# Optimization experiments

Measured on AMD Instinct MI355X. Metric: run time of the kernel, lower is better.

## Reference

```python
import jax, jax.numpy as jnp
import numpy as np

B, S, W = 32, 128, 16
E, CD, H, P = 256, 64, 512, 256
V, CV, NC = 50000, 256, 6
CK, WK = 8, 64  # merged char/word conv kernel sizes


def conv1d(x, w, b):
    # x: [N, Cin, L], w: [Cout, Cin, K] -> [N, Cout, L-K+1] (VALID)
    y = jax.lax.conv_general_dilated(x, w, (1,), 'VALID',
                                     dimension_numbers=('NCH', 'OIH', 'NCH'))
    return y + b[None, :, None]


def setup_inputs() -> dict:
    key = jax.random.key(0)
    ks = iter(jax.random.split(key, 40))
    nrm = lambda shape: jax.random.normal(next(ks), shape, dtype=jnp.float32) * 0.05
    return {
        'seq': jax.random.randint(next(ks), (B, S), 0, V),
        'seq_char': jax.random.randint(next(ks), (B, S, W), 0, CV),
        'classes': jnp.arange(NC, dtype=jnp.int32).reshape(NC, 1),
        'embed_w': nrm((V, E)),
        'char_embed_w': nrm((CV, CD)),
        'class_embed_w': nrm((NC, E)),
        'char_conv_w': nrm((CD, CD, CK)), 'char_conv_b': nrm((CD,)),
        'word_conv_w': nrm((E, E + CD, WK)), 'word_conv_b': nrm((E,)),
        'f_Wih': nrm((4 * H, E + CD)), 'f_Whh': nrm((4 * H, H)), 'f_b': nrm((4 * H,)),
        'b_Wih': nrm((4 * H, E + CD)), 'b_Whh': nrm((4 * H, H)), 'b_b': nrm((4 * H,)),
        'attend': nrm((E, 2 * H)),
        'd_Wih': nrm((6 * H, E + 2 * H)), 'd_Whh': nrm((6 * H, 2 * H)),
        'd_bih': nrm((6 * H,)), 'd_bhh': nrm((6 * H,)),
        'proj_w': nrm((P, 2 * H)), 'proj_b': nrm((P,)),
        'cls_w': nrm((2, P)), 'cls_b': nrm((2,)),
    }


def reference(seq, seq_char, classes, embed_w, char_embed_w, class_embed_w,
              char_conv_w, char_conv_b, word_conv_w, word_conv_b,
              f_Wih, f_Whh, f_b, b_Wih, b_Whh, b_b, attend,
              d_Wih, d_Whh, d_bih, d_bhh, proj_w, proj_b, cls_w, cls_b):
    # eval-mode forward (dropout p=0.01 is identity at eval time)
    Bq, Sq = seq.shape
    pad_mask = (seq > 0).astype(jnp.float32)            # [B,S]
    word_e = jnp.tanh(embed_w[seq])                     # [B,S,E]
    # char CNN: all char convs share kernel size -> merged into one conv
    ce = char_embed_w[seq_char]                         # [B,S,W,CD]
    ce = ce.reshape(Bq * Sq, W, CD).transpose(0, 2, 1)  # [B*S, CD, W]
    char_feat = jnp.tanh(conv1d(ce, char_conv_w, char_conv_b).mean(-1).reshape(Bq, Sq, CD))
    x = jnp.concatenate([word_e, char_feat], -1)        # [B,S,E+CD]
    # word CNN over full sequence -> [B,E]
    conv_seq = jnp.tanh(conv1d(x.transpose(0, 2, 1), word_conv_w, word_conv_b).mean(-1))
    # BiLSTM; backward direction uses seq_emb[-i], i.e. order [0, S-1, ..., 1] (as in original)
    xs = x.transpose(1, 0, 2)                           # [S,B,E+CD]
    xs_b = xs[(-jnp.arange(Sq)) % Sq]

    def lstm_scan(Wih, Whh, b, inputs):
        def step(carry, xt):
            h, c = carry
            g = xt @ Wih.T + h @ Whh.T + b
            i, f, gg, o = jnp.split(g, 4, axis=-1)
            c = jax.nn.sigmoid(f) * c + jax.nn.sigmoid(i) * jnp.tanh(gg)
            h = jax.nn.sigmoid(o) * jnp.tanh(c)
            return (h, c), h
        h0 = jnp.zeros((Bq, H), x.dtype)
        _, hs = jax.lax.scan(step, (h0, h0), inputs)
        return hs

    fouts = lstm_scan(f_Wih, f_Whh, f_b, xs)            # [S,B,H]
    bouts = lstm_scan(b_Wih, b_Whh, b_b, xs_b)[::-1]    # reversed, as in original
    seq_repr = jnp.concatenate([fouts, bouts], -1)      # [S,B,2H]
    h0 = seq_repr[-1]                                   # decoder init state [B,2H]
    seq_repr = seq_repr.transpose(1, 0, 2)              # [B,S,2H]
    # class attention: the expanded attn rows are identical across positions,
    # so sum over dim 1 of the [B,S,S] bmm equals S * tanh(a_c) . seq_repr[b,t]
    a = jnp.tanh(jnp.tanh(class_embed_w[classes[:, 0]])) @ attend   # [C,2H]
    scores = Sq * jnp.einsum('ch,bth->cbt', jnp.tanh(a), seq_repr)  # [C,B,S]
    scores = scores * pad_mask[None]
    att_ctx = jnp.einsum('cbt,bth->cbh', jnp.tanh(scores), seq_repr)  # [C,B,2H]

    def gru_step(h, ctx):
        inp = jnp.concatenate([conv_seq, ctx], -1)      # [B, E+2H]
        gi = inp @ d_Wih.T + d_bih
        gh = h @ d_Whh.T + d_bhh
        ir, iz, inn = jnp.split(gi, 3, -1)
        hr, hz, hn = jnp.split(gh, 3, -1)
        r = jax.nn.sigmoid(ir + hr)
        z = jax.nn.sigmoid(iz + hz)
        n = jnp.tanh(inn + r * hn)
        h_new = jnp.tanh((1 - z) * n + z * h)           # post-tanh state fed back (as in original)
        logits = (h_new @ proj_w.T + proj_b) @ cls_w.T + cls_b
        return h_new, jax.nn.log_softmax(logits, -1)

    _, outs = jax.lax.scan(gru_step, h0, att_ctx)       # [C,B,2]
    return outs
```

## Files before the change

### kernel.cpp

```cpp
#include <hip/hip_runtime.h>

typedef __bf16 bf16_t;
typedef __bf16 bf16x8 __attribute__((ext_vector_type(8)));
typedef float f32x4 __attribute__((ext_vector_type(4)));
typedef unsigned u32x4 __attribute__((ext_vector_type(4)));
typedef unsigned long long u64;

static constexpr int BB = 32, SS = 128, WW = 16, EE = 256, CDm = 64, HH = 512, PP = 256;
static constexpr int EC = 320;
static constexpr int H2 = 1024;
static constexpr int G6 = 3072;
static constexpr int NKT = 28;
static constexpr int NKTX = 12;

__device__ __forceinline__ float sigm(float x){ return 1.f/(1.f + expf(-x)); }

#define ALOAD(p)    __hip_atomic_load((p),  __ATOMIC_RELAXED, __HIP_MEMORY_SCOPE_AGENT)
#define ASTORE(p,v) __hip_atomic_store((p),(v),__ATOMIC_RELAXED, __HIP_MEMORY_SCOPE_AGENT)

template<bool LLC>
__device__ __forceinline__ unsigned ld_flag(const unsigned* p){
  unsigned r;
  if constexpr (LLC)
    asm volatile("global_load_dword %0, %1, off sc0 sc1\n\ts_waitcnt vmcnt(0)"
                 : "=&v"(r) : "v"(p) : "memory");
  else
    asm volatile("global_load_dword %0, %1, off sc0\n\ts_waitcnt vmcnt(0)"
                 : "=&v"(r) : "v"(p) : "memory");
  return r;
}
template<bool LLC>
__device__ __forceinline__ void ld16(u32x4& d, const void* p){
  if constexpr (LLC)
    asm volatile("global_load_dwordx4 %0, %1, off sc0 sc1" : "=&v"(d) : "v"(p) : "memory");
  else
    asm volatile("global_load_dwordx4 %0, %1, off sc0"     : "=&v"(d) : "v"(p) : "memory");
}
template<bool LLC>
__device__ __forceinline__ void st32(unsigned* p, unsigned v){
  if constexpr (LLC)
    asm volatile("global_store_dword %0, %1, off sc0 sc1" :: "v"(p), "v"(v) : "memory");
  else
    asm volatile("global_store_dword %0, %1, off sc0"     :: "v"(p), "v"(v) : "memory");
}
__device__ __forceinline__ void vm_drain(){
  asm volatile("s_waitcnt vmcnt(0)" ::: "memory");
  __builtin_amdgcn_sched_barrier(0);
}

__global__ void k_embed(const int* __restrict__ seq, const float* __restrict__ embed_w,
                        float* __restrict__ x, float* __restrict__ mask){
  int bs = blockIdx.x; int c = threadIdx.x;
  int wid = seq[bs];
  x[(size_t)bs*EC + c] = tanhf(embed_w[(size_t)wid*EE + c]);
  if (c == 0) mask[bs] = (wid > 0) ? 1.f : 0.f;
}

__global__ void k_cbar(const int* __restrict__ seq_char, const float* __restrict__ cemb,
                       float* __restrict__ cbar){
  int bs = blockIdx.x; int c = threadIdx.x;
  float ce[WW];
  #pragma unroll
  for (int p = 0; p < WW; ++p){
    int id = seq_char[bs*WW + p];
    ce[p] = cemb[(size_t)id*CDm + c];
  }
  #pragma unroll
  for (int k = 0; k < 8; ++k){
    float s = 0.f;
    #pragma unroll
    for (int p = 0; p < 9; ++p) s += ce[k+p];
    cbar[(size_t)bs*512 + c*8 + k] = s * (1.f/9.f);
  }
}

__global__ __launch_bounds__(64) void k_xbar(const float* __restrict__ x, float* __restrict__ xbar){
  __shared__ float xl[64][129];
  int gid = blockIdx.x*64 + threadIdx.x;
  int b = gid / EC, c = gid % EC;
  int tl = threadIdx.x;
  for (int t = 0; t < SS; ++t) xl[tl][t] = x[((size_t)b*SS + t)*EC + c];
  float s = 0.f;
  for (int t = 0; t < 65; ++t) s += xl[tl][t];
  const float inv = 1.f/65.f;
  float* o = &xbar[(size_t)(b*EC + c)*64];
  o[0] = s*inv;
  for (int k = 1; k < 64; ++k){ s += xl[tl][k+64] - xl[tl][k-1]; o[k] = s*inv; }
}

template<int BM,int BN,int TM,int TN>
__global__ __launch_bounds__(256) void k_gemm(const float* __restrict__ A,
    const float* __restrict__ Wm, float* __restrict__ part,
    int M, int N, int K, int kslice){
  __shared__ float As[32][BM+4];
  __shared__ float Ws[32][BN+4];
  const int tid = threadIdx.x;
  const int tx = tid & 15, ty = tid >> 4;
  const int m0 = blockIdx.x*BM, n0 = blockIdx.y*BN, ks = blockIdx.z;
  const int kb = ks*kslice;
  float acc[TM][TN];
  #pragma unroll
  for (int i = 0; i < TM; ++i)
    #pragma unroll
    for (int j = 0; j < TN; ++j) acc[i][j] = 0.f;
  for (int kt = 0; kt < kslice; kt += 32){
    constexpr int AIT = (BM*8)/256;
    #pragma unroll
    for (int it = 0; it < AIT; ++it){
      int ch = tid + it*256;
      int r = ch >> 3, kc = (ch & 7)*4;
      float4 v = *(const float4*)(A + (size_t)(m0+r)*K + kb + kt + kc);
      As[kc+0][r]=v.x; As[kc+1][r]=v.y; As[kc+2][r]=v.z; As[kc+3][r]=v.w;
    }
    constexpr int WIT = (BN*8)/256;
    #pragma unroll
    for (int it = 0; it < WIT; ++it){
      int ch = tid + it*256;
      int r = ch >> 3, kc = (ch & 7)*4;
      float4 v = *(const float4*)(Wm + (size_t)(n0+r)*K + kb + kt + kc);
      Ws[kc+0][r]=v.x; Ws[kc+1][r]=v.y; Ws[kc+2][r]=v.z; Ws[kc+3][r]=v.w;
    }
    __syncthreads();
    #pragma unroll
    for (int kk = 0; kk < 32; ++kk){
      float a[TM], wv[TN];
      #pragma unroll
      for (int i = 0; i < TM; ++i) a[i] = As[kk][ty*TM+i];
      #pragma unroll
      for (int j = 0; j < TN; ++j) wv[j] = Ws[kk][tx*TN+j];
      #pragma unroll
      for (int i = 0; i < TM; ++i)
        #pragma unroll
        for (int j = 0; j < TN; ++j) acc[i][j] = fmaf(a[i], wv[j], acc[i][j]);
    }
    __syncthreads();
  }
  #pragma unroll
  for (int i = 0; i < TM; ++i){
    int row = m0 + ty*TM + i;
    #pragma unroll
    for (int j = 0; j < TN; ++j){
      int col = n0 + tx*TN + j;
      part[((size_t)ks*M + row)*N + col] = acc[i][j];
    }
  }
}

__global__ __launch_bounds__(64) void k_fin(const float* __restrict__ part,
    const float* __restrict__ bias, float* __restrict__ out,
    int M, int N, int KS, int ldc, int act){
  int col = blockIdx.x*64 + threadIdx.x;
  int row = blockIdx.y;
  float v = bias ? bias[col] : 0.f;
  for (int ks = 0; ks < KS; ++ks) v += part[((size_t)ks*M + row)*N + col];
  if (act) v = tanhf(v);
  out[(size_t)row*ldc + col] = v;
}

__global__ __launch_bounds__(64) void k_packw(const float* __restrict__ fWih, const float* __restrict__ fWhh,
    const float* __restrict__ bWih, const float* __restrict__ bWhh, bf16_t* __restrict__ Wp){
  int id = blockIdx.x;
  int kt = id % NKT; id /= NKT;
  int slice = id % 32; int dir = id / 32;
  int l = threadIdx.x;
  const float* Whh = dir ? bWhh : fWhh;
  const float* Wih = dir ? bWih : fWih;
  int krow = (l >> 4)*8;
  for (int nt = 0; nt < 4; ++nt){
    int row = nt*512 + slice*16 + (l & 15);
    bf16_t* dst = &Wp[((((size_t)(dir*32+slice)*NKT + kt)*4 + nt)*64 + l)*8];
    if (kt < 16){
      const float* src = &Whh[(size_t)row*512 + kt*32 + krow];
      #pragma unroll
      for (int r = 0; r < 8; ++r) dst[r] = (bf16_t)src[r];
    } else {
      int kx = (kt-16)*32 + krow;
      if (kx + 8 <= 320){
        const float* src = &Wih[(size_t)row*320 + kx];
        #pragma unroll
        for (int r = 0; r < 8; ++r) dst[r] = (bf16_t)src[r];
      } else {
        #pragma unroll
        for (int r = 0; r < 8; ++r) dst[r] = (bf16_t)0.f;
      }
    }
  }
}

__global__ __launch_bounds__(64) void k_packdw(const float* __restrict__ W, bf16_t* __restrict__ Wo){
  int id = blockIdx.x;
  int kt = id % 32; id /= 32;
  int nt = id % 3;  int wg = id / 3;
  int l = threadIdx.x;
  int col = nt*1024 + wg*16 + (l & 15);
  int k0 = kt*32 + (l >> 4)*8;
  bf16_t* dst = Wo + (((size_t)(wg*3 + nt)*32 + kt)*64 + l)*8;
  const float* src = W + (size_t)col*1024 + k0;
  #pragma unroll
  for (int r = 0; r < 8; ++r) dst[r] = (bf16_t)src[r];
}

__global__ __launch_bounds__(64) void k_packpw(const float* __restrict__ W, bf16_t* __restrict__ Wo){
  int id = blockIdx.x;
  int kt = id & 31, wg = id >> 5;
  int l = threadIdx.x;
  int col = wg*16 + (l & 15);
  int k0 = kt*32 + (l >> 4)*8;
  bf16_t* dst = Wo + (((size_t)wg*32 + kt)*64 + l)*8;
  const float* src = W + (size_t)col*1024 + k0;
  #pragma unroll
  for (int r = 0; r < 8; ++r) dst[r] = (bf16_t)src[r];
}

__global__ __launch_bounds__(64) void k_packx(const float* __restrict__ x, bf16_t* __restrict__ xp){
  int id = blockIdx.x;
  int ktx = id % NKTX; id /= NKTX;
  int mt = id & 1; int t = id >> 1;
  int l = threadIdx.x;
  int b = (l & 15) + 16*mt;
  int c = ktx*32 + (l >> 4)*8;
  bf16_t* dst = &xp[(((size_t)t*2 + mt)*NKTX + ktx)*64*8 + (size_t)l*8];
  if (c + 8 <= EC){
    const float* src = &x[((size_t)b*SS + t)*EC + c];
    #pragma unroll
    for (int r = 0; r < 8; ++r) dst[r] = (bf16_t)src[r];
  } else {
    #pragma unroll
    for (int r = 0; r < 8; ++r) dst[r] = (bf16_t)0.f;
  }
}

__global__ __launch_bounds__(256) void k_zero(unsigned int* __restrict__ base, int n){
  int i = blockIdx.x*256 + threadIdx.x;
  if (i < n) ASTORE(base + i, 0u);
}

__global__ __launch_bounds__(64) void k_hprep(const float* __restrict__ seq_repr,
                                              bf16_t* __restrict__ hdp){
  int mt = blockIdx.x >> 5, kt = blockIdx.x & 31, l = threadIdx.x;
  int b = mt*16 + (l & 15);
  int jb = kt*32 + (l >> 4)*8;
  const float* src = &seq_repr[((size_t)b*SS + 127)*H2 + jb];
  unsigned* dst = (unsigned*)(hdp + (((size_t)mt*32 + kt)*64 + l)*8);
  #pragma unroll
  for (int p = 0; p < 4; ++p){
    unsigned pk = (unsigned)__builtin_bit_cast(unsigned short, (bf16_t)src[2*p])
                | ((unsigned)__builtin_bit_cast(unsigned short, (bf16_t)src[2*p+1]) << 16);
    ASTORE(dst + p, pk);
  }
}

template<bool LLC>
__device__ void lstm_body(const bf16_t* __restrict__ Wp, const bf16_t* __restrict__ xp,
    bf16_t* __restrict__ hp, const float* __restrict__ fb, const float* __restrict__ bb,
    float* __restrict__ seq_repr, unsigned* __restrict__ lf,
    int dir, int slice, int tid, bf16_t* Wl, float (*red)[32][65],
    float* bias_l, float (*c_l)[32]){
  const int wv = tid >> 6, lane = tid & 63;
  {
    const uint4* src = (const uint4*)(Wp + ((size_t)(dir*32 + slice))*NKT*4*64*8);
    uint4* dst = (uint4*)Wl;
    for (int i = tid; i < NKT*4*64*8/8; i += 256) dst[i] = src[i];
  }
  if (tid < 64){
    const float* bv = dir ? bb : fb;
    bias_l[tid] = bv[(tid >> 4)*512 + slice*16 + (tid & 15)];
  }
  ((float*)c_l)[tid]       = 0.f;
  ((float*)c_l)[tid + 256] = 0.f;
  __syncthreads();

  for (int t = 0; t < SS; ++t){
    const int ph = t & 1;
    const int s = dir ? ((SS - t) & 127) : t;
    f32x4 acc[2][4];
    f32x4 zero = {0.f,0.f,0.f,0.f};
    #pragma unroll
    for (int m = 0; m < 2; ++m)
      #pragma unroll
      for (int n = 0; n < 4; ++n) acc[m][n] = zero;

    const bf16_t* xb = xp + (size_t)s*2*NKTX*64*8;
    bf16x8 ax[3][2];
    #pragma unroll
    for (int i = 0; i < 3; ++i){
      int ktx = wv*3 + i;
      #pragma unroll
      for (int m = 0; m < 2; ++m)
        ax[i][m] = *reinterpret_cast<const bf16x8*>(xb + (((size_t)m*NKTX + ktx)*64 + lane)*8);
    }
    #pragma unroll
    for (int i = 0; i < 3; ++i){
      int kt = 16 + wv*3 + i;
      #pragma unroll
      for (int nt = 0; nt < 4; ++nt){
        bf16x8 Bf = *reinterpret_cast<const bf16x8*>(&Wl[(((size_t)kt*4 + nt)*64 + lane)*8]);
        acc[0][nt] = __builtin_amdgcn_mfma_f32_16x16x32_bf16(ax[i][0], Bf, acc[0][nt], 0, 0, 0);
        acc[1][nt] = __builtin_amdgcn_mfma_f32_16x16x32_bf16(ax[i][1], Bf, acc[1][nt], 0, 0, 0);
      }
    }
    if (t > 0 && lane < 8){
      int prod = dir*32 + (wv + 4*(lane >> 1))*2 + (lane & 1);
      const unsigned* fp = lf + prod*16;
      unsigned tgt = (unsigned)t;
      for(;;){
        unsigned v = ld_flag<LLC>(fp);
        if (__ballot(v < tgt) == 0ull) break;
      }
    }
    const bf16_t* hb_ = hp + ((size_t)(ph*2 + dir))*2*16*64*8;
    u32x4 hr[4][2];
    #pragma unroll
    for (int i = 0; i < 4; ++i){
      int kt = wv + 4*i;
      #pragma unroll
      for (int m = 0; m < 2; ++m)
        ld16<LLC>(hr[i][m], hb_ + (((size_t)m*16 + kt)*64 + lane)*8);
    }
    vm_drain();
    #pragma unroll
    for (int i = 0; i < 4; ++i){
      int kt = wv + 4*i;
      bf16x8 a0 = __builtin_bit_cast(bf16x8, hr[i][0]);
      bf16x8 a1 = __builtin_bit_cast(bf16x8, hr[i][1]);
      #pragma unroll
      for (int nt = 0; nt < 4; ++nt){
        bf16x8 Bf = *reinterpret_cast<const bf16x8*>(&Wl[(((size_t)kt*4 + nt)*64 + lane)*8]);
        acc[0][nt] = __builtin_amdgcn_mfma_f32_16x16x32_bf16(a0, Bf, acc[0][nt], 0, 0, 0);
        acc[1][nt] = __builtin_amdgcn_mfma_f32_16x16x32_bf16(a1, Bf, acc[1][nt], 0, 0, 0);
      }
    }
    {
      int r0 = (lane >> 4)*4, cc = lane & 15;
      #pragma unroll
      for (int m = 0; m < 2; ++m)
        #pragma unroll
        for (int n = 0; n < 4; ++n)
          #pragma unroll
          for (int e = 0; e < 4; ++e)
            red[wv][m*16 + r0 + e][n*16 + cc] = acc[m][n][e];
    }
    __syncthreads();
    {
      int b = tid & 31, jjp = tid >> 5;
      float hv[2];
      #pragma unroll
      for (int u2 = 0; u2 < 2; ++u2){
        int jj = jjp*2 + u2;
        float gi_ = bias_l[jj],     gf_ = bias_l[16+jj];
        float gg_ = bias_l[32+jj],  go_ = bias_l[48+jj];
        #pragma unroll
        for (int w2 = 0; w2 < 4; ++w2){
          gi_ += red[w2][b][jj];      gf_ += red[w2][b][16+jj];
          gg_ += red[w2][b][32+jj];   go_ += red[w2][b][48+jj];
        }
        float ii = sigm(gi_), ff = sigm(gf_), g2 = tanhf(gg_), oo = sigm(go_);
        float c = ff*c_l[jj][b] + ii*g2;
        c_l[jj][b] = c;
        hv[u2] = oo*tanhf(c);
      }
      int j0 = slice*16 + jjp*2;
      int s_out = dir ? (127 - t) : t;
      float2 st; st.x = hv[0]; st.y = hv[1];
      *(float2*)&seq_repr[((size_t)b*SS + s_out)*H2 + dir*HH + j0] = st;
      int mt = b >> 4, kth = j0 >> 5, ln = (b & 15) + 16*((j0 >> 3) & 3), rg = j0 & 7;
      unsigned pk = (unsigned)__builtin_bit_cast(unsigned short, (bf16_t)hv[0])
                  | ((unsigned)__builtin_bit_cast(unsigned short, (bf16_t)hv[1]) << 16);
      unsigned* dst = (unsigned*)(hp +
          ((((size_t)((ph^1)*2 + dir)*2 + mt)*16 + kth)*64 + ln)*8 + rg);
      st32<LLC>(dst, pk);
    }
    asm volatile("s_waitcnt vmcnt(0)" ::: "memory");
    __syncthreads();
    if (tid == 0)
      st32<LLC>(lf + (dir*32 + slice)*16, (unsigned)(t+1));
  }
}

__global__ __launch_bounds__(256, 1) void k_lstm(const bf16_t* __restrict__ Wp,
    const bf16_t* __restrict__ xp, bf16_t* __restrict__ hp,
    const float* __restrict__ fb, const float* __restrict__ bb,
    float* __restrict__ seq_repr, unsigned* __restrict__ lf,
    unsigned* __restrict__ xcc_tab, unsigned* __restrict__ modep){
  const int blk = blockIdx.x;
  const int tid = threadIdx.x;
  __shared__ __align__(16) bf16_t Wl[NKT*4*64*8];
  __shared__ float red[4][32][65];
  __shared__ float bias_l[64];
  __shared__ float c_l[16][32];
  __shared__ unsigned mode_s;

  unsigned xcc;
  asm volatile("s_getreg_b32 %0, hwreg(HW_REG_XCC_ID)" : "=s"(xcc));
  if (tid == 0) ASTORE(xcc_tab + blk, xcc + 1u);
  if (blk == 0){
    unsigned* tabl = (unsigned*)red;
    unsigned v = 0; int spins = 0;
    for (;;){
      v = ALOAD(xcc_tab + tid);
      if (v != 0u || spins >= 200000) break;
      ++spins; __builtin_amdgcn_s_sleep(2);
    }
    tabl[tid] = v;
    __syncthreads();
    if (tid == 0){
      unsigned mode = 1;
      unsigned c0 = tabl[0], c1 = tabl[1];
      if (c0 == 0u || c1 == 0u) mode = 2;
      for (int k = 0; k < 32; ++k)
        if (tabl[8*k] != c0 || tabl[8*k + 1] != c1) mode = 2;
      ASTORE(modep, mode);
      mode_s = mode;
    }
    __syncthreads();
  } else {
    if (tid == 0){
      unsigned m;
      while ((m = ALOAD(modep)) == 0u) __builtin_amdgcn_s_sleep(2);
      mode_s = m;
    }
    __syncthreads();
  }
  const unsigned mode = mode_s;
  int dir, slice; bool worker;
  if (mode == 1){ worker = (blk & 7) < 2; dir = blk & 7; slice = blk >> 3; }
  else          { worker = blk < 64;      dir = blk >> 5; slice = blk & 31; }
  if (!worker) return;
  if (mode == 1)
    lstm_body<false>(Wp, xp, hp, fb, bb, seq_repr, lf, dir, slice, tid, Wl, red, bias_l, c_l);
  else
    lstm_body<true >(Wp, xp, hp, fb, bb, seq_repr, lf, dir, slice, tid, Wl, red, bias_l, c_l);
}

__global__ __launch_bounds__(256) void k_ta(const int* __restrict__ classes,
    const float* __restrict__ cls_emb, const float* __restrict__ attend, float* __restrict__ ta){
  int c = blockIdx.x;
  __shared__ float t2[EE];
  int tid = threadIdx.x;
  int ci = classes[c];
  t2[tid] = tanhf(tanhf(cls_emb[(size_t)ci*EE + tid]));
  __syncthreads();
  for (int r = 0; r < 4; ++r){
    int h = r*256 + tid;
    float acc = 0.f;
    for (int e = 0; e < EE; ++e) acc = fmaf(t2[e], attend[(size_t)e*H2 + h], acc);
    ta[c*H2 + h] = tanhf(acc);
  }
}

__global__ __launch_bounds__(256) void k_ctx(const float* __restrict__ ta,
    const float* __restrict__ seq_repr, const float* __restrict__ mask, float* __restrict__ ctx){
  int c = blockIdx.x, b = blockIdx.y;
  __shared__ float ta_l[H2];
  __shared__ float ps[128][2];
  __shared__ float sc[128];
  int tid = threadIdx.x;
  for (int i = tid; i < H2; i += 256) ta_l[i] = ta[c*H2 + i];
  __syncthreads();
  {
    int tt = tid >> 1, half = tid & 1;
    const float* row = &seq_repr[((size_t)b*SS + tt)*H2 + half*512];
    const float* tl = &ta_l[half*512];
    float p = 0.f;
    for (int i = 0; i < 512; i += 4){
      float4 v = *(const float4*)&row[i];
      p = fmaf(tl[i], v.x, p);   p = fmaf(tl[i+1], v.y, p);
      p = fmaf(tl[i+2], v.z, p); p = fmaf(tl[i+3], v.w, p);
    }
    ps[tt][half] = p;
  }
  __syncthreads();
  if (tid < 128){
    float s = (ps[tid][0] + ps[tid][1]) * 128.f * mask[b*SS + tid];
    sc[tid] = tanhf(s);
  }
  __syncthreads();
  {
    int h = tid*4;
    float4 a = {0.f,0.f,0.f,0.f};
    for (int t = 0; t < SS; ++t){
      float s = sc[t];
      float4 v = *(const float4*)&seq_repr[((size_t)b*SS + t)*H2 + h];
      a.x = fmaf(s, v.x, a.x); a.y = fmaf(s, v.y, a.y);
      a.z = fmaf(s, v.z, a.z); a.w = fmaf(s, v.w, a.w);
    }
    *(float4*)&ctx[((size_t)c*BB + b)*H2 + h] = a;
  }
}

__global__ void k_inp(const float* __restrict__ conv_seq, const float* __restrict__ ctx,
                      float* __restrict__ inp){
  int cb = blockIdx.x;
  int b = cb & 31;
  for (int k = threadIdx.x; k < 1280; k += 256){
    float v = (k < 256) ? conv_seq[b*256 + k] : ctx[(size_t)cb*H2 + (k - 256)];
    inp[(size_t)cb*1280 + k] = v;
  }
}

__global__ __launch_bounds__(256, 1) void k_dec(
    const bf16_t* __restrict__ Whp, const bf16_t* __restrict__ Ppw,
    const float* __restrict__ gi, const float* __restrict__ d_bhh,
    const float* __restrict__ seq_repr,
    const float* __restrict__ proj_b, const float* __restrict__ cls_w,
    const float* __restrict__ cls_b, bf16_t* __restrict__ hdp,
    float* __restrict__ pl, unsigned int* __restrict__ dfh,
    unsigned int* __restrict__ dfpl, float* __restrict__ out){
  const int wg = blockIdx.x;
  const int tid = threadIdx.x;
  const int wv = tid >> 6, lane = tid & 63;
  __shared__ __align__(16) bf16_t Wl[3*32*64*8];
  __shared__ float red[4][32][49];
  __shared__ float plred[8][32][2];
  __shared__ float cv[2];
  {
    const uint4* src = (const uint4*)(Whp + (size_t)wg*3*32*64*8);
    uint4* dst = (uint4*)Wl;
    for (int i = tid; i < 3*32*64*8/8; i += 256) dst[i] = src[i];
  }
  const int b = tid & 31, jp = tid >> 5;
  const int j0 = wg*16 + jp*2;
  float hold[2];
  hold[0] = seq_repr[((size_t)b*SS + 127)*H2 + j0];
  hold[1] = seq_repr[((size_t)b*SS + 127)*H2 + j0 + 1];
  float bhh[3][2];
  #pragma unroll
  for (int g = 0; g < 3; ++g){
    bhh[g][0] = d_bhh[g*1024 + j0];
    bhh[g][1] = d_bhh[g*1024 + j0 + 1];
  }
  __syncthreads();
  union HU { unsigned long long u[2]; bf16x8 v; };
  const int r0 = (lane >> 4)*4, cc = lane & 15;

  for (int c = 0; c < 6; ++c){
    if (c > 0){
      const unsigned int* fp = dfh + lane*16;
      unsigned tgt = (unsigned)c;
      for(;;){
        unsigned v = ALOAD(fp);
        if (__ballot(v < tgt) == 0ull) break;
      }
    }
    f32x4 acc[2][3];
    f32x4 zero = {0.f,0.f,0.f,0.f};
    #pragma unroll
    for (int m = 0; m < 2; ++m)
      #pragma unroll
      for (int n = 0; n < 3; ++n) acc[m][n] = zero;
    const bf16_t* hb = hdp + (size_t)(c & 1)*2*32*64*8;
    #pragma unroll
    for (int i = 0; i < 8; ++i){
      int kt = wv*8 + i;
      HU u0, u1;
      const unsigned long long* p0 = (const unsigned long long*)(hb + (((size_t)0*32 + kt)*64 + lane)*8);
      const unsigned long long* p1 = (const unsigned long long*)(hb + (((size_t)1*32 + kt)*64 + lane)*8);
      u0.u[0] = ALOAD(p0);     u0.u[1] = ALOAD(p0 + 1);
      u1.u[0] = ALOAD(p1);     u1.u[1] = ALOAD(p1 + 1);
      #pragma unroll
      for (int nt = 0; nt < 3; ++nt){
        bf16x8 Bf = *reinterpret_cast<const bf16x8*>(&Wl[(((size_t)nt*32 + kt)*64 + lane)*8]);
        acc[0][nt] = __builtin_amdgcn_mfma_f32_16x16x32_bf16(u0.v, Bf, acc[0][nt], 0, 0, 0);
        acc[1][nt] = __builtin_amdgcn_mfma_f32_16x16x32_bf16(u1.v, Bf, acc[1][nt], 0, 0, 0);
      }
    }
    #pragma unroll
    for (int m = 0; m < 2; ++m)
      #pragma unroll
      for (int n = 0; n < 3; ++n)
        #pragma unroll
        for (int e = 0; e < 4; ++e)
          red[wv][m*16 + r0 + e][n*16 + cc] = acc[m][n][e];
    __syncthreads();
    float hnew[2];
    #pragma unroll
    for (int u2 = 0; u2 < 2; ++u2){
      int jj = jp*2 + u2;
      float r_ = 0.f, z_ = 0.f, n_ = 0.f;
      #pragma unroll
      for (int w = 0; w < 4; ++w){
        r_ += red[w][b][jj]; z_ += red[w][b][16+jj]; n_ += red[w][b][32+jj];
      }
      const float* gr = gi + ((size_t)(c*BB) + b)*G6 + wg*16 + jj;
      float rr = sigm(gr[0]    + bhh[0][u2] + r_);
      float zz = sigm(gr[1024] + bhh[1][u2] + z_);
      float nn = tanhf(gr[2048] + rr*(bhh[2][u2] + n_));
      hnew[u2] = tanhf((1.f - zz)*nn + zz*hold[u2]);
      hold[u2] = hnew[u2];
    }
    {
      int kt = j0 >> 5, ln = (b & 15) + 16*((j0 >> 3) & 3), rg = j0 & 7, mt = b >> 4;
      unsigned pk = (unsigned)__builtin_bit_cast(unsigned short, (bf16_t)hnew[0])
                  | ((unsigned)__builtin_bit_cast(unsigned short, (bf16_t)hnew[1]) << 16);
      unsigned* dst = (unsigned*)(hdp + (size_t)((c+1)&1)*2*32*64*8 +
                                  (((size_t)(mt*32 + kt)*64 + ln)*8 + rg));
      ASTORE(dst, pk);
    }
    __syncthreads();
    if (tid == 0)
      ASTORE(dfh + wg*16, (unsigned)(c+1));
    if (wg < 16){
      {
        const unsigned int* fp = dfh + lane*16;
        unsigned tgt = (unsigned)(c+1);
        for(;;){
          unsigned v = ALOAD(fp);
          if (__ballot(v < tgt) == 0ull) break;
        }
      }
      f32x4 pacc[2] = {zero, zero};
      const bf16_t* hb2 = hdp + (size_t)((c+1)&1)*2*32*64*8;
      #pragma unroll
      for (int i = 0; i < 8; ++i){
        int kt = wv*8 + i;
        HU u0, u1;
        const unsigned long long* p0 = (const unsigned long long*)(hb2 + (((size_t)0*32 + kt)*64 + lane)*8);
        const unsigned long long* p1 = (const unsigned long long*)(hb2 + (((size_t)1*32 + kt)*64 + lane)*8);
        u0.u[0] = ALOAD(p0);     u0.u[1] = ALOAD(p0 + 1);
        u1.u[0] = ALOAD(p1);     u1.u[1] = ALOAD(p1 + 1);
        bf16x8 Bf = *reinterpret_cast<const bf16x8*>(Ppw + (((size_t)wg*32 + kt)*64 + lane)*8);
        pacc[0] = __builtin_amdgcn_mfma_f32_16x16x32_bf16(u0.v, Bf, pacc[0], 0, 0, 0);
        pacc[1] = __builtin_amdgcn_mfma_f32_16x16x32_bf16(u1.v, Bf, pacc[1], 0, 0, 0);
      }
      #pragma unroll
      for (int m = 0; m < 2; ++m)
        #pragma unroll
        for (int e = 0; e < 4; ++e)
          red[wv][m*16 + r0 + e][cc] = pacc[m][e];
      __syncthreads();
      {
        int colp = tid >> 5;
        float v0 = 0.f, v1 = 0.f;
        #pragma unroll
        for (int w = 0; w < 4; ++w){
          v0 += red[w][b][colp*2];
          v1 += red[w][b][colp*2+1];
        }
        int c0 = wg*16 + colp*2, c1 = c0 + 1;
        plred[colp][b][0] = v0*cls_w[c0]      + v1*cls_w[c1];
        plred[colp][b][1] = v0*cls_w[PP + c0] + v1*cls_w[PP + c1];
      }
      __syncthreads();
      if (tid < 32){
        float s0 = 0.f, s1 = 0.f;
        #pragma unroll
        for (int g = 0; g < 8; ++g){ s0 += plred[g][tid][0]; s1 += plred[g][tid][1]; }
        unsigned* dp = (unsigned*)(pl + (((size_t)c*16 + wg)*32 + tid)*2);
        ASTORE(dp,     __builtin_bit_cast(unsigned, s0));
        ASTORE(dp + 1, __builtin_bit_cast(unsigned, s1));
      }
      __syncthreads();
      if (tid == 0)
        ASTORE(dfpl + wg*16, (unsigned)(c+1));
    }
  }
  if (wg == 0){
    if (lane < 16){
      const unsigned int* fp = dfpl + lane*16;
      for(;;){
        unsigned v = ALOAD(fp);
        if (__ballot(v < 6u) == 0ull) break;
      }
    }
    __syncthreads();
    float* cr = (float*)red;
    cr[tid*2]   = proj_b[tid]*cls_w[tid];
    cr[tid*2+1] = proj_b[tid]*cls_w[PP + tid];
    __syncthreads();
    if (tid < 2){
      float s = 0.f;
      for (int i = 0; i < 256; ++i) s += cr[i*2 + tid];
      cv[tid] = s;
    }
    __syncthreads();
    if (tid < 32){
      for (int c = 0; c < 6; ++c){
        float a0 = cv[0] + cls_b[0], a1 = cv[1] + cls_b[1];
        for (int w = 0; w < 16; ++w){
          const unsigned* dp = (const unsigned*)(pl + (((size_t)c*16 + w)*32 + tid)*2);
          a0 += __builtin_bit_cast(float, ALOAD(dp));
          a1 += __builtin_bit_cast(float, ALOAD(dp + 1));
        }
        float mx = fmaxf(a0, a1);
        float ls = mx + logf(expf(a0 - mx) + expf(a1 - mx));
        out[((size_t)c*BB + tid)*2 + 0] = a0 - ls;
        out[((size_t)c*BB + tid)*2 + 1] = a1 - ls;
      }
    }
  }
}

extern "C" void kernel_launch(void* const* d_in, const int* in_sizes, int n_in,
                              void* d_out, int out_size, void* d_ws, size_t ws_size,
                              hipStream_t stream){
  const int*   seq          = (const int*)  d_in[0];
  const int*   seq_char     = (const int*)  d_in[1];
  const int*   classes      = (const int*)  d_in[2];
  const float* embed_w      = (const float*)d_in[3];
  const float* char_embed_w = (const float*)d_in[4];
  const float* class_embed_w= (const float*)d_in[5];
  const float* char_conv_w  = (const float*)d_in[6];
  const float* char_conv_b  = (const float*)d_in[7];
  const float* word_conv_w  = (const float*)d_in[8];
  const float* word_conv_b  = (const float*)d_in[9];
  const float* f_Wih = (const float*)d_in[10];
  const float* f_Whh = (const float*)d_in[11];
  const float* f_b   = (const float*)d_in[12];
  const float* b_Wih = (const float*)d_in[13];
  const float* b_Whh = (const float*)d_in[14];
  const float* b_b   = (const float*)d_in[15];
  const float* attend = (const float*)d_in[16];
  const float* d_Wih  = (const float*)d_in[17];
  const float* d_Whh  = (const float*)d_in[18];
  const float* d_bih  = (const float*)d_in[19];
  const float* d_bhh  = (const float*)d_in[20];
  const float* proj_w = (const float*)d_in[21];
  const float* proj_b = (const float*)d_in[22];
  const float* cls_w  = (const float*)d_in[23];
  const float* cls_b  = (const float*)d_in[24];
  float* out = (float*)d_out;

  char* wsb = (char*)d_ws;
  size_t off = 0;
  auto alloc = [&](size_t bytes) -> char* {
    char* p = wsb + off;
    off += (bytes + 255) & ~(size_t)255;
    return p;
  };
  unsigned int* flags = (unsigned int*)alloc(12288);
  unsigned int* lf   = flags;
  unsigned int* dfh  = flags + 1024;
  unsigned int* dfpl = flags + 2048;
  unsigned int* xcc_tab = (unsigned int*)alloc(1024);
  unsigned int* modep   = (unsigned int*)alloc(256);
  bf16_t* hp  = (bf16_t*)alloc((size_t)2*2*2*16*64*8 * 2);
  const int ZERO_DWORDS = 3072 + 256 + 64 + 32768;
  bf16_t* hdp = (bf16_t*)alloc((size_t)2*2*32*64*8 * 2);
  bf16_t* Wp  = (bf16_t*)alloc((size_t)2*32*NKT*4*64*8 * 2);
  bf16_t* Whp = (bf16_t*)alloc((size_t)64*3*32*64*8 * 2);
  bf16_t* Ppw = (bf16_t*)alloc((size_t)16*32*64*8 * 2);
  bf16_t* xp  = (bf16_t*)alloc((size_t)128*2*NKTX*64*8 * 2);
  float* pl       = (float*)alloc((size_t)6*16*32*2*4);
  float* x        = (float*)alloc((size_t)BB*SS*EC*4);
  float* mask     = (float*)alloc((size_t)BB*SS*4);
  float* cbar     = (float*)alloc((size_t)4096*512*4);
  float* xbar     = (float*)alloc((size_t)BB*EC*64*4);
  float* conv_seq = (float*)alloc((size_t)BB*256*4);
  float* seq_repr = (float*)alloc((size_t)BB*SS*H2*4);
  float* ta       = (float*)alloc((size_t)6*H2*4);
  float* ctx      = (float*)alloc((size_t)6*BB*H2*4);
  float* inp      = (float*)alloc((size_t)192*1280*4);
  float* gi       = (float*)alloc((size_t)192*G6*4);
  float* part_char= (float*)alloc((size_t)2*4096*64*4);
  float* part_word= (float*)alloc((size_t)32*BB*256*4);
  float* part_gi  = (float*)alloc((size_t)4*192*G6*4);
  (void)ws_size; (void)in_sizes; (void)n_in; (void)out_size;

  k_zero<<<(ZERO_DWORDS + 255)/256, 256, 0, stream>>>((unsigned int*)d_ws, ZERO_DWORDS);

  k_packw<<<2*32*NKT, 64, 0, stream>>>(f_Wih, f_Whh, b_Wih, b_Whh, Wp);
  k_packdw<<<64*3*32, 64, 0, stream>>>(d_Whh, Whp);
  k_packpw<<<16*32, 64, 0, stream>>>(proj_w, Ppw);
  k_embed<<<BB*SS, 256, 0, stream>>>(seq, embed_w, x, mask);
  k_cbar<<<BB*SS, 64, 0, stream>>>(seq_char, char_embed_w, cbar);
  k_gemm<32,64,2,4><<<dim3(128,1,2), 256, 0, stream>>>(cbar, char_conv_w, part_char, 4096, 64, 512, 256);
  k_fin<<<dim3(1,4096), 64, 0, stream>>>(part_char, char_conv_b, x + 256, 4096, 64, 2, EC, 1);
  k_xbar<<<160, 64, 0, stream>>>(x, xbar);
  k_gemm<32,64,2,4><<<dim3(1,4,32), 256, 0, stream>>>(xbar, word_conv_w, part_word, 32, 256, 20480, 640);
  k_fin<<<dim3(4,32), 64, 0, stream>>>(part_word, word_conv_b, conv_seq, 32, 256, 32, 256, 1);
  k_packx<<<128*2*NKTX, 64, 0, stream>>>(x, xp);
  k_lstm<<<256, 256, 0, stream>>>(Wp, xp, hp, f_b, b_b, seq_repr, lf, xcc_tab, modep);
  k_ta<<<6, 256, 0, stream>>>(classes, class_embed_w, attend, ta);
  k_ctx<<<dim3(6,32), 256, 0, stream>>>(ta, seq_repr, mask, ctx);
  k_inp<<<192, 256, 0, stream>>>(conv_seq, ctx, inp);
  k_gemm<64,64,4,4><<<dim3(3,48,4), 256, 0, stream>>>(inp, d_Wih, part_gi, 192, G6, 1280, 320);
  k_fin<<<dim3(48,192), 64, 0, stream>>>(part_gi, d_bih, gi, 192, G6, 4, G6, 0);
  k_hprep<<<64, 64, 0, stream>>>(seq_repr, hdp);
  k_dec<<<64, 256, 0, stream>>>(Whp, Ppw, gi, d_bhh, seq_repr, proj_b, cls_w, cls_b,
                                hdp, pl, dfh, dfpl, out);
}
```

Before: 645.1 us.

## Restructure LSTM recurrence into 128 single-wave workgroups with wave-local gating

The bidirectional LSTM kernel now runs as 128 one-wave workgroups, each owning 8 hidden units per direction, instead of 64 four-wave blocks with 16 units each. Each wave computes the full K reduction itself, so the cross-wave shared-memory reduction and __syncthreads per step go away, and the cell state stays in registers. The XCC-detection mode switch and its non-LLC path are removed: all flag and h loads/stores now use system-coherent sc0 sc1, and the spin-wait adds s_sleep. The trade-off is waiting on 64 producer flags per step instead of 16, and a serial 28-tile MFMA chain in a single wave.

Result: slower. 1.007 ms (+56.2%).

```diff
diff --git a/kernel.cpp b/kernel.cpp
--- a/kernel.cpp
+++ b/kernel.cpp
@@ -18,30 +18,20 @@
 #define ALOAD(p)    __hip_atomic_load((p),  __ATOMIC_RELAXED, __HIP_MEMORY_SCOPE_AGENT)
 #define ASTORE(p,v) __hip_atomic_store((p),(v),__ATOMIC_RELAXED, __HIP_MEMORY_SCOPE_AGENT)
 
-template<bool LLC>
 __device__ __forceinline__ unsigned ld_flag(const unsigned* p){
   unsigned r;
-  if constexpr (LLC)
-    asm volatile("global_load_dword %0, %1, off sc0 sc1\n\ts_waitcnt vmcnt(0)"
-                 : "=&v"(r) : "v"(p) : "memory");
-  else
-    asm volatile("global_load_dword %0, %1, off sc0\n\ts_waitcnt vmcnt(0)"
-                 : "=&v"(r) : "v"(p) : "memory");
+  asm volatile("global_load_dword %0, %1, off sc0 sc1\n\ts_waitcnt vmcnt(0)"
+               : "=&v"(r) : "v"(p) : "memory");
   return r;
 }
-template<bool LLC>
 __device__ __forceinline__ void ld16(u32x4& d, const void* p){
-  if constexpr (LLC)
-    asm volatile("global_load_dwordx4 %0, %1, off sc0 sc1" : "=&v"(d) : "v"(p) : "memory");
-  else
-    asm volatile("global_load_dwordx4 %0, %1, off sc0"     : "=&v"(d) : "v"(p) : "memory");
-}
-template<bool LLC>
-__device__ __forceinline__ void st32(unsigned* p, unsigned v){
-  if constexpr (LLC)
-    asm volatile("global_store_dword %0, %1, off sc0 sc1" :: "v"(p), "v"(v) : "memory");
-  else
-    asm volatile("global_store_dword %0, %1, off sc0"     :: "v"(p), "v"(v) : "memory");
+  asm volatile("global_load_dwordx4 %0, %1, off sc0 sc1" : "=&v"(d) : "v"(p) : "memory");
+}
+__device__ __forceinline__ void st16(void* p, u32x4 v){
+  asm volatile("global_store_dwordx4 %0, %1, off sc0 sc1" :: "v"(p), "v"(v) : "memory");
+}
+__device__ __forceinline__ void st32c(unsigned* p, unsigned v){
+  asm volatile("global_store_dword %0, %1, off sc0 sc1" :: "v"(p), "v"(v) : "memory");
 }
 __device__ __forceinline__ void vm_drain(){
   asm volatile("s_waitcnt vmcnt(0)" ::: "memory");
@@ -157,18 +147,19 @@
   out[(size_t)row*ldc + col] = v;
 }
 
-__global__ __launch_bounds__(64) void k_packw(const float* __restrict__ fWih, const float* __restrict__ fWhh,
-    const float* __restrict__ bWih, const float* __restrict__ bWhh, bf16_t* __restrict__ Wp){
+__global__ __launch_bounds__(64) void k_packw2(const float* __restrict__ fWih, const float* __restrict__ fWhh,
+    const float* __restrict__ bWih, const float* __restrict__ bWhh, bf16_t* __restrict__ Wp2){
   int id = blockIdx.x;
   int kt = id % NKT; id /= NKT;
-  int slice = id % 32; int dir = id / 32;
+  int ub = id % 64; int dir = id / 64;
   int l = threadIdx.x;
   const float* Whh = dir ? bWhh : fWhh;
   const float* Wih = dir ? bWih : fWih;
+  int cl = l & 15, ul = cl >> 2, g = cl & 3;
   int krow = (l >> 4)*8;
-  for (int nt = 0; nt < 4; ++nt){
-    int row = nt*512 + slice*16 + (l & 15);
-    bf16_t* dst = &Wp[((((size_t)(dir*32+slice)*NKT + kt)*4 + nt)*64 + l)*8];
+  for (int nt = 0; nt < 2; ++nt){
+    int row = g*512 + ub*8 + nt*4 + ul;
+    bf16_t* dst = &Wp2[((((size_t)(dir*64+ub)*NKT + kt)*2 + nt)*64 + l)*8];
     if (kt < 16){
       const float* src = &Whh[(size_t)row*512 + kt*32 + krow];
       #pragma unroll
@@ -250,186 +241,123 @@
   }
 }
 
-template<bool LLC>
-__device__ void lstm_body(const bf16_t* __restrict__ Wp, const bf16_t* __restrict__ xp,
-    bf16_t* __restrict__ hp, const float* __restrict__ fb, const float* __restrict__ bb,
-    float* __restrict__ seq_repr, unsigned* __restrict__ lf,
-    int dir, int slice, int tid, bf16_t* Wl, float (*red)[32][65],
-    float* bias_l, float (*c_l)[32]){
-  const int wv = tid >> 6, lane = tid & 63;
+__global__ __launch_bounds__(64, 1) void k_lstm(const bf16_t* __restrict__ Wp2,
+    const bf16_t* __restrict__ xp, bf16_t* __restrict__ hp,
+    const float* __restrict__ fb, const float* __restrict__ bb,
+    float* __restrict__ seq_repr, unsigned* __restrict__ lf){
+  const int wg = blockIdx.x;
+  const int dir = wg >> 6, ub = wg & 63;
+  const int lane = threadIdx.x;
+  __shared__ __align__(16) bf16_t Wl[NKT*2*64*8];
+  __shared__ float red[32*33 + 1];
+  __shared__ __align__(16) bf16_t tr[32*8];
+
   {
-    const uint4* src = (const uint4*)(Wp + ((size_t)(dir*32 + slice))*NKT*4*64*8);
+    const uint4* src = (const uint4*)(Wp2 + ((size_t)(dir*64 + ub))*NKT*2*64*8);
     uint4* dst = (uint4*)Wl;
-    for (int i = tid; i < NKT*4*64*8/8; i += 256) dst[i] = src[i];
-  }
-  if (tid < 64){
+    #pragma unroll
+    for (int i = 0; i < 56; ++i) dst[lane + i*64] = src[lane + i*64];
+  }
+  const int gb = lane & 31;
+  const int up = lane >> 5;
+  float bias[16];
+  {
     const float* bv = dir ? bb : fb;
-    bias_l[tid] = bv[(tid >> 4)*512 + slice*16 + (tid & 15)];
-  }
-  ((float*)c_l)[tid]       = 0.f;
-  ((float*)c_l)[tid + 256] = 0.f;
+    #pragma unroll
+    for (int g = 0; g < 4; ++g)
+      #pragma unroll
+      for (int k = 0; k < 4; ++k)
+        bias[g*4 + k] = bv[g*512 + ub*8 + up + 2*k];
+  }
+  float cst[4] = {0.f, 0.f, 0.f, 0.f};
+  const int wri = (lane & 3)*8 + ((lane >> 2) & 3);
+  const int wboff = (lane >> 4)*4;
   __syncthreads();
 
   for (int t = 0; t < SS; ++t){
     const int ph = t & 1;
     const int s = dir ? ((SS - t) & 127) : t;
-    f32x4 acc[2][4];
-    f32x4 zero = {0.f,0.f,0.f,0.f};
-    #pragma unroll
-    for (int m = 0; m < 2; ++m)
-      #pragma unroll
-      for (int n = 0; n < 4; ++n) acc[m][n] = zero;
-
+    f32x4 acc[2][2];
+    {
+      f32x4 z = {0.f,0.f,0.f,0.f};
+      acc[0][0]=z; acc[0][1]=z; acc[1][0]=z; acc[1][1]=z;
+    }
     const bf16_t* xb = xp + (size_t)s*2*NKTX*64*8;
-    bf16x8 ax[3][2];
-    #pragma unroll
-    for (int i = 0; i < 3; ++i){
-      int ktx = wv*3 + i;
-      #pragma unroll
-      for (int m = 0; m < 2; ++m)
-        ax[i][m] = *reinterpret_cast<const bf16x8*>(xb + (((size_t)m*NKTX + ktx)*64 + lane)*8);
-    }
-    #pragma unroll
-    for (int i = 0; i < 3; ++i){
-      int kt = 16 + wv*3 + i;
-      #pragma unroll
-      for (int nt = 0; nt < 4; ++nt){
-        bf16x8 Bf = *reinterpret_cast<const bf16x8*>(&Wl[(((size_t)kt*4 + nt)*64 + lane)*8]);
-        acc[0][nt] = __builtin_amdgcn_mfma_f32_16x16x32_bf16(ax[i][0], Bf, acc[0][nt], 0, 0, 0);
-        acc[1][nt] = __builtin_amdgcn_mfma_f32_16x16x32_bf16(ax[i][1], Bf, acc[1][nt], 0, 0, 0);
-      }
-    }
-    if (t > 0 && lane < 8){
-      int prod = dir*32 + (wv + 4*(lane >> 1))*2 + (lane & 1);
-      const unsigned* fp = lf + prod*16;
+    #pragma unroll
+    for (int i = 0; i < NKTX; ++i){
+      bf16x8 a0 = *reinterpret_cast<const bf16x8*>(xb + (((size_t)0*NKTX + i)*64 + lane)*8);
+      bf16x8 a1 = *reinterpret_cast<const bf16x8*>(xb + (((size_t)1*NKTX + i)*64 + lane)*8);
+      #pragma unroll
+      for (int nt = 0; nt < 2; ++nt){
+        bf16x8 Bf = *reinterpret_cast<const bf16x8*>(&Wl[((((size_t)(16+i))*2 + nt)*64 + lane)*8]);
+        acc[0][nt] = __builtin_amdgcn_mfma_f32_16x16x32_bf16(a0, Bf, acc[0][nt], 0, 0, 0);
+        acc[1][nt] = __builtin_amdgcn_mfma_f32_16x16x32_bf16(a1, Bf, acc[1][nt], 0, 0, 0);
+      }
+    }
+    if (t > 0){
+      const unsigned* fp = lf + ((size_t)(dir*64 + lane))*16;
       unsigned tgt = (unsigned)t;
       for(;;){
-        unsigned v = ld_flag<LLC>(fp);
+        unsigned v = ld_flag(fp);
         if (__ballot(v < tgt) == 0ull) break;
-      }
-    }
-    const bf16_t* hb_ = hp + ((size_t)(ph*2 + dir))*2*16*64*8;
-    u32x4 hr[4][2];
-    #pragma unroll
-    for (int i = 0; i < 4; ++i){
-      int kt = wv + 4*i;
-      #pragma unroll
-      for (int m = 0; m < 2; ++m)
-        ld16<LLC>(hr[i][m], hb_ + (((size_t)m*16 + kt)*64 + lane)*8);
+        __builtin_amdgcn_s_sleep(1);
+      }
+    }
+    const bf16_t* hb = hp + ((size_t)(ph*2 + dir))*2*16*64*8;
+    u32x4 hr[16][2];
+    #pragma unroll
+    for (int i = 0; i < 16; ++i){
+      ld16(hr[i][0], hb + (((size_t)0*16 + i)*64 + lane)*8);
+      ld16(hr[i][1], hb + (((size_t)1*16 + i)*64 + lane)*8);
     }
     vm_drain();
     #pragma unroll
-    for (int i = 0; i < 4; ++i){
-      int kt = wv + 4*i;
+    for (int i = 0; i < 16; ++i){
       bf16x8 a0 = __builtin_bit_cast(bf16x8, hr[i][0]);
       bf16x8 a1 = __builtin_bit_cast(bf16x8, hr[i][1]);
       #pragma unroll
-      for (int nt = 0; nt < 4; ++nt){
-        bf16x8 Bf = *reinterpret_cast<const bf16x8*>(&Wl[(((size_t)kt*4 + nt)*64 + lane)*8]);
+      for (int nt = 0; nt < 2; ++nt){
+        bf16x8 Bf = *reinterpret_cast<const bf16x8*>(&Wl[(((size_t)i*2 + nt)*64 + lane)*8]);
         acc[0][nt] = __builtin_amdgcn_mfma_f32_16x16x32_bf16(a0, Bf, acc[0][nt], 0, 0, 0);
         acc[1][nt] = __builtin_amdgcn_mfma_f32_16x16x32_bf16(a1, Bf, acc[1][nt], 0, 0, 0);
       }
     }
+    #pragma unroll
+    for (int m = 0; m < 2; ++m)
+      #pragma unroll
+      for (int nt = 0; nt < 2; ++nt)
+        *(f32x4*)&red[(wri + nt*4)*33 + wboff + 16*m] = acc[m][nt];
+    float hv[4];
+    #pragma unroll
+    for (int k = 0; k < 4; ++k){
+      int uu = up + 2*k;
+      float gi_ = red[(0*8 + uu)*33 + gb] + bias[0*4 + k];
+      float gf_ = red[(1*8 + uu)*33 + gb] + bias[1*4 + k];
+      float gg_ = red[(2*8 + uu)*33 + gb] + bias[2*4 + k];
+      float go_ = red[(3*8 + uu)*33 + gb] + bias[3*4 + k];
+      float ii = sigm(gi_), ff = sigm(gf_), g2 = tanhf(gg_), oo = sigm(go_);
+      float c = ff*cst[k] + ii*g2;
+      cst[k] = c;
+      hv[k] = oo*tanhf(c);
+      tr[gb*8 + uu] = (bf16_t)hv[k];
+    }
+    if (lane < 32){
+      int m = lane >> 4, bg = lane & 15;
+      u32x4 v = *(const u32x4*)&tr[(bg + 16*m)*8];
+      bf16_t* dsth = hp + ((((size_t)((ph^1)*2 + dir)*2 + m)*16 + (ub >> 2))*64
+                     + (bg + 16*(ub & 3)))*8;
+      st16(dsth, v);
+    }
+    vm_drain();
+    if (lane == 0)
+      st32c(lf + ((size_t)(dir*64 + ub))*16, (unsigned)(t+1));
     {
-      int r0 = (lane >> 4)*4, cc = lane & 15;
-      #pragma unroll
-      for (int m = 0; m < 2; ++m)
-        #pragma unroll
-        for (int n = 0; n < 4; ++n)
-          #pragma unroll
-          for (int e = 0; e < 4; ++e)
-            red[wv][m*16 + r0 + e][n*16 + cc] = acc[m][n][e];
-    }
-    __syncthreads();
-    {
-      int b = tid & 31, jjp = tid >> 5;
-      float hv[2];
-      #pragma unroll
-      for (int u2 = 0; u2 < 2; ++u2){
-        int jj = jjp*2 + u2;
-        float gi_ = bias_l[jj],     gf_ = bias_l[16+jj];
-        float gg_ = bias_l[32+jj],  go_ = bias_l[48+jj];
-        #pragma unroll
-        for (int w2 = 0; w2 < 4; ++w2){
-          gi_ += red[w2][b][jj];      gf_ += red[w2][b][16+jj];
-          gg_ += red[w2][b][32+jj];   go_ += red[w2][b][48+jj];
-        }
-        float ii = sigm(gi_), ff = sigm(gf_), g2 = tanhf(gg_), oo = sigm(go_);
-        float c = ff*c_l[jj][b] + ii*g2;
-        c_l[jj][b] = c;
-        hv[u2] = oo*tanhf(c);
-      }
-      int j0 = slice*16 + jjp*2;
       int s_out = dir ? (127 - t) : t;
-      float2 st; st.x = hv[0]; st.y = hv[1];
-      *(float2*)&seq_repr[((size_t)b*SS + s_out)*H2 + dir*HH + j0] = st;
-      int mt = b >> 4, kth = j0 >> 5, ln = (b & 15) + 16*((j0 >> 3) & 3), rg = j0 & 7;
-      unsigned pk = (unsigned)__builtin_bit_cast(unsigned short, (bf16_t)hv[0])
-                  | ((unsigned)__builtin_bit_cast(unsigned short, (bf16_t)hv[1]) << 16);
-      unsigned* dst = (unsigned*)(hp +
-          ((((size_t)((ph^1)*2 + dir)*2 + mt)*16 + kth)*64 + ln)*8 + rg);
-      st32<LLC>(dst, pk);
-    }
-    asm volatile("s_waitcnt vmcnt(0)" ::: "memory");
-    __syncthreads();
-    if (tid == 0)
-      st32<LLC>(lf + (dir*32 + slice)*16, (unsigned)(t+1));
-  }
-}
-
-__global__ __launch_bounds__(256, 1) void k_lstm(const bf16_t* __restrict__ Wp,
-    const bf16_t* __restrict__ xp, bf16_t* __restrict__ hp,
-    const float* __restrict__ fb, const float* __restrict__ bb,
-    float* __restrict__ seq_repr, unsigned* __restrict__ lf,
-    unsigned* __restrict__ xcc_tab, unsigned* __restrict__ modep){
-  const int blk = blockIdx.x;
-  const int tid = threadIdx.x;
-  __shared__ __align__(16) bf16_t Wl[NKT*4*64*8];
-  __shared__ float red[4][32][65];
-  __shared__ float bias_l[64];
-  __shared__ float c_l[16][32];
-  __shared__ unsigned mode_s;
-
-  unsigned xcc;
-  asm volatile("s_getreg_b32 %0, hwreg(HW_REG_XCC_ID)" : "=s"(xcc));
-  if (tid == 0) ASTORE(xcc_tab + blk, xcc + 1u);
-  if (blk == 0){
-    unsigned* tabl = (unsigned*)red;
-    unsigned v = 0; int spins = 0;
-    for (;;){
-      v = ALOAD(xcc_tab + tid);
-      if (v != 0u || spins >= 200000) break;
-      ++spins; __builtin_amdgcn_s_sleep(2);
-    }
-    tabl[tid] = v;
-    __syncthreads();
-    if (tid == 0){
-      unsigned mode = 1;
-      unsigned c0 = tabl[0], c1 = tabl[1];
-      if (c0 == 0u || c1 == 0u) mode = 2;
-      for (int k = 0; k < 32; ++k)
-        if (tabl[8*k] != c0 || tabl[8*k + 1] != c1) mode = 2;
-      ASTORE(modep, mode);
-      mode_s = mode;
-    }
-    __syncthreads();
-  } else {
-    if (tid == 0){
-      unsigned m;
-      while ((m = ALOAD(modep)) == 0u) __builtin_amdgcn_s_sleep(2);
-      mode_s = m;
-    }
-    __syncthreads();
-  }
-  const unsigned mode = mode_s;
-  int dir, slice; bool worker;
-  if (mode == 1){ worker = (blk & 7) < 2; dir = blk & 7; slice = blk >> 3; }
-  else          { worker = blk < 64;      dir = blk >> 5; slice = blk & 31; }
-  if (!worker) return;
-  if (mode == 1)
-    lstm_body<false>(Wp, xp, hp, fb, bb, seq_repr, lf, dir, slice, tid, Wl, red, bias_l, c_l);
-  else
-    lstm_body<true >(Wp, xp, hp, fb, bb, seq_repr, lf, dir, slice, tid, Wl, red, bias_l, c_l);
+      float* so = &seq_repr[((size_t)gb*SS + s_out)*H2 + dir*HH + ub*8 + up];
+      #pragma unroll
+      for (int k = 0; k < 4; ++k) so[2*k] = hv[k];
+    }
+  }
 }
 
 __global__ __launch_bounds__(256) void k_ta(const int* __restrict__ classes,
@@ -727,16 +655,14 @@
     off += (bytes + 255) & ~(size_t)255;
     return p;
   };
-  unsigned int* flags = (unsigned int*)alloc(12288);
+  unsigned int* flags = (unsigned int*)alloc(16384);
   unsigned int* lf   = flags;
-  unsigned int* dfh  = flags + 1024;
-  unsigned int* dfpl = flags + 2048;
-  unsigned int* xcc_tab = (unsigned int*)alloc(1024);
-  unsigned int* modep   = (unsigned int*)alloc(256);
+  unsigned int* dfh  = flags + 2048;
+  unsigned int* dfpl = flags + 3072;
   bf16_t* hp  = (bf16_t*)alloc((size_t)2*2*2*16*64*8 * 2);
-  const int ZERO_DWORDS = 3072 + 256 + 64 + 32768;
+  const int ZERO_DWORDS = 4096 + 32768;
   bf16_t* hdp = (bf16_t*)alloc((size_t)2*2*32*64*8 * 2);
-  bf16_t* Wp  = (bf16_t*)alloc((size_t)2*32*NKT*4*64*8 * 2);
+  bf16_t* Wp2 = (bf16_t*)alloc((size_t)2*64*NKT*2*64*8 * 2);
   bf16_t* Whp = (bf16_t*)alloc((size_t)64*3*32*64*8 * 2);
   bf16_t* Ppw = (bf16_t*)alloc((size_t)16*32*64*8 * 2);
   bf16_t* xp  = (bf16_t*)alloc((size_t)128*2*NKTX*64*8 * 2);
@@ -758,7 +684,7 @@
 
   k_zero<<<(ZERO_DWORDS + 255)/256, 256, 0, stream>>>((unsigned int*)d_ws, ZERO_DWORDS);
 
-  k_packw<<<2*32*NKT, 64, 0, stream>>>(f_Wih, f_Whh, b_Wih, b_Whh, Wp);
+  k_packw2<<<2*64*NKT, 64, 0, stream>>>(f_Wih, f_Whh, b_Wih, b_Whh, Wp2);
   k_packdw<<<64*3*32, 64, 0, stream>>>(d_Whh, Whp);
   k_packpw<<<16*32, 64, 0, stream>>>(proj_w, Ppw);
   k_embed<<<BB*SS, 256, 0, stream>>>(seq, embed_w, x, mask);
@@ -769,7 +695,7 @@
   k_gemm<32,64,2,4><<<dim3(1,4,32), 256, 0, stream>>>(xbar, word_conv_w, part_word, 32, 256, 20480, 640);
   k_fin<<<dim3(4,32), 64, 0, stream>>>(part_word, word_conv_b, conv_seq, 32, 256, 32, 256, 1);
   k_packx<<<128*2*NKTX, 64, 0, stream>>>(x, xp);
-  k_lstm<<<256, 256, 0, stream>>>(Wp, xp, hp, f_b, b_b, seq_repr, lf, xcc_tab, modep);
+  k_lstm<<<128, 64, 0, stream>>>(Wp2, xp, hp, f_b, b_b, seq_repr, lf);
   k_ta<<<6, 256, 0, stream>>>(classes, class_embed_w, attend, ta);
   k_ctx<<<dim3(6,32), 256, 0, stream>>>(ta, seq_repr, mask, ctx);
   k_inp<<<192, 256, 0, stream>>>(conv_seq, ctx, inp);
```
